# Performance work log

Hardware: AMD Instinct MI355X
Metric: run time of the kernel (lower is better)

The kernel has to match this reference:

```python
import jax, jax.numpy as jnp
import numpy as np


def setup_inputs() -> dict:
    key = jax.random.key(0)
    k1, k2 = jax.random.split(key)
    surfaces = jax.random.normal(k1, (4, 4096, 3), dtype=jnp.float32)   # [S, N, K]
    targets = jax.random.normal(k2, (16384, 3), dtype=jnp.float32)      # [M, K]
    return {"surfaces": surfaces, "targets": targets}


def reference(surfaces, targets):
    # Pairwise squared distances ||a-b||^2 = ||a||^2 + ||b||^2 - 2 a.b
    # surfaces: [S, N, K], targets: [M, K]
    a2 = jnp.sum(surfaces * surfaces, axis=-1)          # [S, N]
    b2 = jnp.sum(targets * targets, axis=-1)            # [M]
    ab = jnp.einsum('snk,mk->snm', surfaces, targets)   # [S, N, M]
    dist = a2[:, :, None] + b2[None, None, :] - 2.0 * ab  # [S, N, M]
    # direction='cloud2nearest' -> dim=0: min over surface points N per target
    nearest = jnp.min(dist, axis=1)                     # [S, M]
    # stack over surfaces then min over dim 0 (S)
    nearest = jnp.min(nearest, axis=0)                  # [M]
    return jnp.sum(nearest)
```

## Files before the change

### kernel.cpp

```cpp
#include <hip/hip_runtime.h>
#include <cfloat>


namespace {
constexpr int M   = 16384;
constexpr int SN  = 16384;
constexpr int NCH = 32;
constexpr int PPC = SN / NCH;
constexpr int NG  = 128;
constexpr int TPG = 128;
constexpr int K2B = 256;
}

typedef short bf16x8 __attribute__((ext_vector_type(8)));
typedef float f32x4  __attribute__((ext_vector_type(4)));

static __device__ __forceinline__ unsigned short f2bf(float f) {
  unsigned int u = __builtin_bit_cast(unsigned int, f);
  return (unsigned short)((u + 0x7FFFu + ((u >> 16) & 1u)) >> 16);
}
static __device__ __forceinline__ float bf2f(unsigned short h) {
  unsigned int u = ((unsigned int)h) << 16;
  return __builtin_bit_cast(float, u);
}

__global__ __launch_bounds__(256) void build_ab(
    const float* __restrict__ surf, const float* __restrict__ tgt,
    unsigned short* __restrict__ Aex, unsigned short* __restrict__ Bex,
    float* __restrict__ b2f, unsigned* __restrict__ counter)
{
  const int i = blockIdx.x * 256 + threadIdx.x;
  if (i == 0) counter[0] = 0u;

  {
    const float x = surf[(size_t)i*3+0], y = surf[(size_t)i*3+1], z = surf[(size_t)i*3+2];
    const float s2 = fmaf(x, x, fmaf(y, y, z * z));
    unsigned short row[32];
#pragma unroll
    for (int k = 0; k < 32; ++k) row[k] = 0;
    const float cs[3] = {x, y, z};
#pragma unroll
    for (int c = 0; c < 3; ++c) {
      const unsigned short hi = f2bf(cs[c]);
      const unsigned short lo = f2bf(cs[c] - bf2f(hi));
      row[3*c+0] = hi; row[3*c+1] = hi; row[3*c+2] = lo;
    }
    const unsigned short shi = f2bf(s2);
    const unsigned short slo = f2bf(s2 - bf2f(shi));
    row[9] = shi; row[10] = slo;
#pragma unroll
    for (int k = 0; k < 16; ++k)
      ((unsigned int*)(Aex + (size_t)i*32))[k] =
          (unsigned int)row[2*k] | ((unsigned int)row[2*k+1] << 16);
  }
  {
    const float a = tgt[(size_t)i*3+0], b = tgt[(size_t)i*3+1], c = tgt[(size_t)i*3+2];
    b2f[i] = fmaf(a, a, fmaf(b, b, c * c));
    const float us[3] = {-2.0f*a, -2.0f*b, -2.0f*c};
    unsigned short row[32];
#pragma unroll
    for (int k = 0; k < 32; ++k) row[k] = 0;
#pragma unroll
    for (int q = 0; q < 3; ++q) {
      const unsigned short hi = f2bf(us[q]);
      const unsigned short lo = f2bf(us[q] - bf2f(hi));
      row[3*q+0] = hi; row[3*q+1] = lo; row[3*q+2] = hi;
    }
    const unsigned short one = f2bf(1.0f);
    row[9] = one; row[10] = one;
#pragma unroll
    for (int k = 0; k < 16; ++k)
      ((unsigned int*)(Bex + (size_t)i*32))[k] =
          (unsigned int)row[2*k] | ((unsigned int)row[2*k+1] << 16);
  }
}

__global__ __launch_bounds__(256, 4) void dist_mfma(
    const unsigned short* __restrict__ Aex,
    const unsigned short* __restrict__ Bex,
    float* __restrict__ wmin)
{
  const int tid  = threadIdx.x;
  const int lane = tid & 63;
  const int wid  = tid >> 6;
  const int wg   = blockIdx.x * 4 + wid;
  const int g    = wg & (NG - 1);
  const int c    = wg >> 7;
  const int m0   = g * TPG;
  const int r15  = lane & 15;
  const int koff = (lane >> 4) * 8;

  bf16x8 bfr[8];
#pragma unroll
  for (int f = 0; f < 8; ++f)
    bfr[f] = *(const bf16x8*)(Bex + ((size_t)(m0 + f*16 + r15)) * 32 + koff);

  float mn[8];
#pragma unroll
  for (int f = 0; f < 8; ++f) mn[f] = FLT_MAX;

  const int pbase = c * PPC;
  const unsigned short* ap = Aex + ((size_t)(pbase + r15)) * 32 + koff;

  bf16x8 acur = *(const bf16x8*)ap;
  for (int r = 0; r < PPC / 16; ++r) {
    const int rn = (r + 1 < PPC / 16) ? r + 1 : r;
    const bf16x8 anxt = *(const bf16x8*)(ap + (size_t)rn * 16 * 32);
#pragma unroll
    for (int f = 0; f < 8; ++f) {
      const f32x4 d = __builtin_amdgcn_mfma_f32_16x16x32_bf16(
          acur, bfr[f], (f32x4){0.f, 0.f, 0.f, 0.f}, 0, 0, 0);
      mn[f] = fminf(fminf(mn[f], fminf(d[0], d[1])), fminf(d[2], d[3]));
    }
    acur = anxt;
  }

#pragma unroll
  for (int f = 0; f < 8; ++f) {
    float v = mn[f];
    v = fminf(v, __shfl_xor(v, 16, 64));
    v = fminf(v, __shfl_xor(v, 32, 64));
    mn[f] = v;
  }
  if (lane < 16) {
#pragma unroll
    for (int f = 0; f < 8; ++f)
      wmin[(size_t)c * M + m0 + f * 16 + lane] = mn[f];
  }
}

__global__ __launch_bounds__(256) void dist_min_sum(
    const float* __restrict__ wmin,
    const float* __restrict__ b2f,
    float* __restrict__ part,
    unsigned* __restrict__ counter,
    float* __restrict__ out)
{
  const int tid  = threadIdx.x;
  const int lane = tid & 63;
  const int w    = tid >> 6;
  const int m    = blockIdx.x * 64 + lane;

  float mnv = FLT_MAX;
  const int c0 = w * (NCH / 4);
#pragma unroll
  for (int ci = 0; ci < NCH / 4; ++ci)
    mnv = fminf(mnv, wmin[(size_t)(c0 + ci) * M + m]);

  __shared__ float red[4][64];
  red[w][lane] = mnv;
  __syncthreads();

  if (w == 0) {
    float v = fminf(fminf(red[0][lane], red[1][lane]),
                    fminf(red[2][lane], red[3][lane]));
    v += b2f[m];
    for (int off = 32; off; off >>= 1) v += __shfl_down(v, off, 64);

    unsigned done = 0;
    if (lane == 0) {
      part[blockIdx.x] = v;
      __threadfence();
      done = atomicAdd(counter, 1u);
    }
    done = __shfl(done, 0, 64);

    if (done == (unsigned)(K2B - 1)) {
      __threadfence();
      float s = 0.0f;
#pragma unroll
      for (int i = 0; i < K2B / 64; ++i) s += part[i * 64 + lane];
      for (int off = 32; off; off >>= 1) s += __shfl_down(s, off, 64);
      if (lane == 0) out[0] = s;
    }
  }
}

extern "C" void kernel_launch(void* const* d_in, const int* in_sizes, int n_in,
                              void* d_out, int out_size, void* d_ws, size_t ws_size,
                              hipStream_t stream) {
  const float* surf = (const float*)d_in[0];
  const float* tgt  = (const float*)d_in[1];
  float* out = (float*)d_out;

  unsigned short* Aex = (unsigned short*)d_ws;
  unsigned short* Bex = Aex + (size_t)SN * 32;
  float* b2f  = (float*)(Bex + (size_t)M * 32);
  float* wmin = b2f + M;
  float* part = wmin + (size_t)NCH * M;
  unsigned* counter = (unsigned*)(part + K2B);

  build_ab<<<SN / 256, 256, 0, stream>>>(surf, tgt, Aex, Bex, b2f, counter);
  dist_mfma<<<(NG * NCH) / 4, 256, 0, stream>>>(Aex, Bex, wmin);
  dist_min_sum<<<K2B, 256, 0, stream>>>(wmin, b2f, part, counter, out);
}
```

Before: 40.44 us.

## Widen per-wave target tile to 256 and double-buffer A fragment loads

Each wave now holds 16 B fragments (256 targets) instead of 8, so every loaded A fragment feeds twice as many MFMAs and the grid has half as many waves. The A loop is unrolled by two with loads issued two steps ahead, and the min update uses a three-input min form. Occupancy bounds drop to 2 blocks per SM to make room for the larger register footprint, which leaves fewer waves to hide latency.

```diff
diff --git a/kernel.cpp b/kernel.cpp
--- a/kernel.cpp
+++ b/kernel.cpp
@@ -7,8 +7,9 @@
 constexpr int SN  = 16384;
 constexpr int NCH = 32;
 constexpr int PPC = SN / NCH;
-constexpr int NG  = 128;
-constexpr int TPG = 128;
+constexpr int NG  = 64;
+constexpr int TPG = 256;
+constexpr int FR  = 16;
 constexpr int K2B = 256;
 }
 
@@ -22,6 +23,9 @@
 static __device__ __forceinline__ float bf2f(unsigned short h) {
   unsigned int u = ((unsigned int)h) << 16;
   return __builtin_bit_cast(float, u);
+}
+static __device__ __forceinline__ float min3f(float a, float b, float c) {
+  return fminf(fminf(a, b), c);
 }
 
 __global__ __launch_bounds__(256) void build_ab(
@@ -75,7 +79,7 @@
   }
 }
 
-__global__ __launch_bounds__(256, 4) void dist_mfma(
+__global__ __launch_bounds__(256, 2) void dist_mfma(
     const unsigned short* __restrict__ Aex,
     const unsigned short* __restrict__ Bex,
     float* __restrict__ wmin)
@@ -85,38 +89,49 @@
   const int wid  = tid >> 6;
   const int wg   = blockIdx.x * 4 + wid;
   const int g    = wg & (NG - 1);
-  const int c    = wg >> 7;
+  const int c    = wg >> 6;
   const int m0   = g * TPG;
   const int r15  = lane & 15;
   const int koff = (lane >> 4) * 8;
 
-  bf16x8 bfr[8];
-#pragma unroll
-  for (int f = 0; f < 8; ++f)
+  bf16x8 bfr[FR];
+#pragma unroll
+  for (int f = 0; f < FR; ++f)
     bfr[f] = *(const bf16x8*)(Bex + ((size_t)(m0 + f*16 + r15)) * 32 + koff);
 
-  float mn[8];
-#pragma unroll
-  for (int f = 0; f < 8; ++f) mn[f] = FLT_MAX;
-
-  const int pbase = c * PPC;
-  const unsigned short* ap = Aex + ((size_t)(pbase + r15)) * 32 + koff;
-
-  bf16x8 acur = *(const bf16x8*)ap;
-  for (int r = 0; r < PPC / 16; ++r) {
-    const int rn = (r + 1 < PPC / 16) ? r + 1 : r;
-    const bf16x8 anxt = *(const bf16x8*)(ap + (size_t)rn * 16 * 32);
-#pragma unroll
-    for (int f = 0; f < 8; ++f) {
-      const f32x4 d = __builtin_amdgcn_mfma_f32_16x16x32_bf16(
-          acur, bfr[f], (f32x4){0.f, 0.f, 0.f, 0.f}, 0, 0, 0);
-      mn[f] = fminf(fminf(mn[f], fminf(d[0], d[1])), fminf(d[2], d[3]));
-    }
-    acur = anxt;
-  }
-
-#pragma unroll
-  for (int f = 0; f < 8; ++f) {
+  float mn[FR];
+#pragma unroll
+  for (int f = 0; f < FR; ++f) mn[f] = FLT_MAX;
+
+  const unsigned short* ap = Aex + ((size_t)(c * PPC + r15)) * 32 + koff;
+
+#define LD_A(r)  (*(const bf16x8*)(ap + (size_t)(r) * 16 * 32))
+#define COMPUTE(AT)                                                        \
+  {                                                                        \
+    _Pragma("unroll")                                                      \
+    for (int f = 0; f < FR; ++f) {                                         \
+      const f32x4 d = __builtin_amdgcn_mfma_f32_16x16x32_bf16(             \
+          AT, bfr[f], (f32x4){0.f, 0.f, 0.f, 0.f}, 0, 0, 0);               \
+      mn[f] = min3f(mn[f], fminf(d[0], d[1]), fminf(d[2], d[3]));          \
+    }                                                                      \
+  }
+
+  bf16x8 a0 = LD_A(0);
+  bf16x8 a1 = LD_A(1);
+  for (int r = 0; r < PPC / 16; r += 2) {
+    const int r2 = (r + 2 < PPC / 16) ? r + 2 : PPC / 16 - 1;
+    const int r3 = (r + 3 < PPC / 16) ? r + 3 : PPC / 16 - 1;
+    bf16x8 a2 = LD_A(r2);
+    COMPUTE(a0);
+    bf16x8 a3 = LD_A(r3);
+    COMPUTE(a1);
+    a0 = a2; a1 = a3;
+  }
+#undef COMPUTE
+#undef LD_A
+
+#pragma unroll
+  for (int f = 0; f < FR; ++f) {
     float v = mn[f];
     v = fminf(v, __shfl_xor(v, 16, 64));
     v = fminf(v, __shfl_xor(v, 32, 64));
@@ -124,7 +139,7 @@
   }
   if (lane < 16) {
 #pragma unroll
-    for (int f = 0; f < 8; ++f)
+    for (int f = 0; f < FR; ++f)
       wmin[(size_t)c * M + m0 + f * 16 + lane] = mn[f];
   }
 }
```

Result: slower. 44.61 us (+10.3%).
